# Kernel tuning notes

Measured on AMD Instinct MI355X. Metric: run time of the kernel, lower is better.

## Reference

```python
import jax, jax.numpy as jnp
import numpy as np

EPS = 0.01
BETA = 0.8
GAMMA_A = 0.01
GAMMA_W = 0.01
ALPHA = 1.0
N_UNITS = 128

def setup_inputs() -> dict:
    key = jax.random.key(0)
    ks = jax.random.split(key, 7)
    B, T, D_in, C_out = 512, 1024, 64, 10
    return {
        "x": jax.random.normal(ks[0], (B, T, D_in), dtype=jnp.float32),
        "E_w": jax.random.normal(ks[1], (N_UNITS, D_in), dtype=jnp.float32) / np.sqrt(D_in),
        "E_b": jax.random.normal(ks[2], (N_UNITS,), dtype=jnp.float32) * 0.01,
        "B_p": jax.random.normal(ks[3], (N_UNITS, N_UNITS), dtype=jnp.float32) / N_UNITS,
        "C_p": jax.random.normal(ks[4], (N_UNITS, N_UNITS), dtype=jnp.float32) / N_UNITS,
        "D_w": jax.random.normal(ks[5], (C_out, N_UNITS), dtype=jnp.float32) / np.sqrt(N_UNITS),
        "D_b": jax.random.normal(ks[6], (C_out,), dtype=jnp.float32) * 0.01,
    }

def reference(x, E_w, E_b, B_p, C_p, D_w, D_b):
    B, T, _ = x.shape
    I = jnp.eye(N_UNITS, dtype=x.dtype)
    # Skew/symmetric mixture recurrent matrices (computed once, as in i==0 branch)
    A = BETA * (B_p - B_p.T) + (1.0 - BETA) * (B_p + B_p.T) - GAMMA_A * I
    W = BETA * (C_p - C_p.T) + (1.0 - BETA) * (C_p + C_p.T) - GAMMA_W * I
    # Input projection for all timesteps at once: [T, B, n_units]
    Z = jnp.einsum('bti,ui->tbu', x, E_w) + E_b
    h0 = jnp.zeros((B, N_UNITS), dtype=x.dtype)

    def step(h, z):
        h_update = ALPHA * (h @ A) + jnp.tanh(h @ W + z)
        return h + EPS * h_update, None

    h_final, _ = jax.lax.scan(step, h0, Z)
    return h_final @ D_w.T + D_b
```

## Files before the change

### kernel.cpp

```cpp
#include <hip/hip_runtime.h>

#define EPS_C 0.01f
#define NU    128
#define DIN   64
#define COUT  10
#define TSCALE 2.8853900817779268f

typedef float    f32x4 __attribute__((ext_vector_type(4)));
typedef _Float16 f16x2 __attribute__((ext_vector_type(2)));
typedef _Float16 f16x4 __attribute__((ext_vector_type(4)));
typedef _Float16 f16x8 __attribute__((ext_vector_type(8)));

#define MFMA32(A, B, C) __builtin_amdgcn_mfma_f32_16x16x32_f16((A), (B), (C), 0, 0, 0)
#define BAR() asm volatile("s_waitcnt lgkmcnt(0)\n\ts_barrier" ::: "memory")

__global__ __launch_bounds__(256, 1)
void rnn_core(const float* __restrict__ x,
              const float* __restrict__ E_w, const float* __restrict__ E_b,
              const float* __restrict__ B_p, const float* __restrict__ C_p,
              const float* __restrict__ D_w, const float* __restrict__ D_b,
              float* __restrict__ out, int T)
{
    const int tid  = threadIdx.x;
    const int lane = tid & 63;
    const int w    = tid >> 6;
    const int lid  = lane & 15;
    const int q    = lane >> 4;
    const int g    = blockIdx.x;

    __shared__ __attribute__((aligned(16))) _Float16 xs[2][8 * 1024];
    __shared__ __attribute__((aligned(16))) _Float16 hbuf[2][4][64][8];
    __shared__ float hfin[16][NU + 4];

    f16x8 AT[2][4], WT[2][4], EF[2][2];
    f32x4 ebv[2];
    #pragma unroll
    for (int mt = 0; mt < 2; ++mt) {
        const int m = w * 32 + mt * 16 + lid;
        #pragma unroll
        for (int kt = 0; kt < 4; ++kt) {
            f16x8 fa, fw;
            #pragma unroll
            for (int j = 0; j < 8; ++j) {
                const int k  = kt * 32 + q * 8 + j;
                const float dg = (k == m) ? 0.01f : 0.0f;
                fa[j] = (_Float16)(B_p[k * NU + m] - 0.6f * B_p[m * NU + k] - dg);
                fw[j] = (_Float16)((C_p[k * NU + m] - 0.6f * C_p[m * NU + k] - dg) * TSCALE);
            }
            AT[mt][kt] = fa;  WT[mt][kt] = fw;
        }
        #pragma unroll
        for (int kt = 0; kt < 2; ++kt) {
            f16x8 fe;
            #pragma unroll
            for (int j = 0; j < 8; ++j)
                fe[j] = (_Float16)(E_w[m * DIN + kt * 32 + q * 8 + j] * TSCALE);
            EF[mt][kt] = fe;
        }
        #pragma unroll
        for (int r = 0; r < 4; ++r)
            ebv[mt][r] = E_b[w * 32 + mt * 16 + q * 4 + r] * TSCALE;
    }

    const int bb = tid & 15;
    const int s2 = tid >> 4;
    const float* xrow = x + ((size_t)(g * 16 + bb) * T) * DIN + s2 * 4;
    const int wb2 = (((s2 >> 3) * 64) + (((s2 >> 1) & 3) * 16) + bb) * 16 + (s2 & 1) * 8;

    float4 xg[8];

#define STAGE_WRITE(BUF)                                                      \
    {                                                                         \
        char* base_ = (char*)&xs[(BUF)][0];                                   \
        _Pragma("unroll")                                                     \
        for (int i2 = 0; i2 < 8; ++i2) {                                      \
            float4 v_ = xg[i2];                                               \
            f16x4 h4_;                                                        \
            h4_[0] = (_Float16)v_.x; h4_[1] = (_Float16)v_.y;                 \
            h4_[2] = (_Float16)v_.z; h4_[3] = (_Float16)v_.w;                 \
            *(f16x4*)(base_ + i2 * 2048 + wb2) = h4_;                         \
        }                                                                     \
    }

    ((float4*)&hbuf[0][0][0][0])[tid] = (float4){0.f, 0.f, 0.f, 0.f};
    #pragma unroll
    for (int i = 0; i < 8; ++i)
        xg[i] = *(const float4*)(xrow + (size_t)i * DIN);
    STAGE_WRITE(0)
    __syncthreads();

    char* xsb = (char*)&xs[0][0] + lane * 16;
    char* hrb = (char*)&hbuf[0][0][0][0] + lane * 16;
    char* hwb = (char*)&hbuf[0][0][0][0]
              + (w * 64 + (q >> 1) * 16 + lid) * 16 + (q & 1) * 8;

    f32x4 hf[2] = {{0.f,0.f,0.f,0.f}, {0.f,0.f,0.f,0.f}};
    f32x4 zc0, zc1;
    {
        f16x8 x0 = *(const f16x8*)(xsb);
        f16x8 x1 = *(const f16x8*)(xsb + 1024);
        zc0 = ebv[0];
        zc0 = MFMA32(EF[0][0], x0, zc0);
        zc0 = MFMA32(EF[0][1], x1, zc0);
        zc1 = ebv[1];
        zc1 = MFMA32(EF[1][0], x0, zc1);
        zc1 = MFMA32(EF[1][1], x1, zc1);
    }

    const int nch = T >> 3;
    for (int c = 0; c < nch; ++c) {
        if (c + 1 < nch) {
            const float* xr2 = xrow + (size_t)(c + 1) * 8 * DIN;
            #pragma unroll
            for (int i = 0; i < 8; ++i)
                xg[i] = *(const float4*)(xr2 + (size_t)i * DIN);
        }
        #pragma unroll
        for (int i = 0; i < 8; ++i) {
            const int t  = c * 8 + i;
            const int p  = i & 1;
            const int np = p ^ 1;

            f16x8 hB[4];
            #pragma unroll
            for (int kt = 0; kt < 4; ++kt)
                hB[kt] = *(const f16x8*)(hrb + p * 4096 + kt * 1024);

            int tt = t + 1; if (tt >= T) tt = T - 1;
            char* xb = xsb + ((tt >> 3) & 1) * 16384 + (tt & 7) * 2048;
            f16x8 xfA = *(const f16x8*)(xb);
            f16x8 xfB = *(const f16x8*)(xb + 1024);

            f32x4 wa0 = zc0, wa1 = zc1;
            #pragma unroll
            for (int kt = 0; kt < 4; ++kt) {
                wa0 = MFMA32(WT[0][kt], hB[kt], wa0);
                wa1 = MFMA32(WT[1][kt], hB[kt], wa1);
            }

            float rc[2][4];
            #pragma unroll
            for (int r = 0; r < 4; ++r) {
                rc[0][r] = __builtin_amdgcn_rcpf(__builtin_amdgcn_exp2f(wa0[r]) + 1.0f);
                rc[1][r] = __builtin_amdgcn_rcpf(__builtin_amdgcn_exp2f(wa1[r]) + 1.0f);
            }

            #pragma unroll
            for (int kt = 0; kt < 4; ++kt) {
                hf[0] = MFMA32(AT[0][kt], hB[kt], hf[0]);
                hf[1] = MFMA32(AT[1][kt], hB[kt], hf[1]);
            }
            f32x4 zn0 = ebv[0], zn1 = ebv[1];
            zn0 = MFMA32(EF[0][0], xfA, zn0);
            zn1 = MFMA32(EF[1][0], xfA, zn1);
            zn0 = MFMA32(EF[0][1], xfB, zn0);
            zn1 = MFMA32(EF[1][1], xfB, zn1);

            #pragma unroll
            for (int mt = 0; mt < 2; ++mt) {
                #pragma unroll
                for (int r = 0; r < 4; ++r)
                    hf[mt][r] = __builtin_fmaf(-2.0f, rc[mt][r], hf[mt][r] + 1.0f);
                f16x2 lo = __builtin_bit_cast(f16x2,
                    __builtin_amdgcn_cvt_pkrtz(EPS_C * hf[mt][0], EPS_C * hf[mt][1]));
                f16x2 hi = __builtin_bit_cast(f16x2,
                    __builtin_amdgcn_cvt_pkrtz(EPS_C * hf[mt][2], EPS_C * hf[mt][3]));
                f16x4 nh;
                nh[0] = lo[0]; nh[1] = lo[1]; nh[2] = hi[0]; nh[3] = hi[1];
                *(f16x4*)(hwb + np * 4096 + mt * 512) = nh;
            }
            zc0 = zn0; zc1 = zn1;

            if (i == 5 && c + 1 < nch) STAGE_WRITE((c + 1) & 1)
            BAR();
        }
    }

    #pragma unroll
    for (int mt = 0; mt < 2; ++mt)
        #pragma unroll
        for (int r = 0; r < 4; ++r)
            hfin[lid][w * 32 + mt * 16 + q * 4 + r] = EPS_C * hf[mt][r];
    __syncthreads();

    if (tid < 16 * COUT) {
        const int r  = tid / COUT;
        const int cc = tid - r * COUT;
        float acc = D_b[cc];
        #pragma unroll 8
        for (int u = 0; u < NU; ++u)
            acc = fmaf(hfin[r][u], D_w[cc * NU + u], acc);
        out[((size_t)g * 16 + r) * COUT + cc] = acc;
    }
}

extern "C" void kernel_launch(void* const* d_in, const int* in_sizes, int n_in,
                              void* d_out, int out_size, void* d_ws, size_t ws_size,
                              hipStream_t stream)
{
    const float* x   = (const float*)d_in[0];
    const float* E_w = (const float*)d_in[1];
    const float* E_b = (const float*)d_in[2];
    const float* B_p = (const float*)d_in[3];
    const float* C_p = (const float*)d_in[4];
    const float* D_w = (const float*)d_in[5];
    const float* D_b = (const float*)d_in[6];
    float* out = (float*)d_out;

    const int B  = out_size / COUT;
    const int T  = in_sizes[0] / (B * DIN);
    const int NB = B / 16;

    rnn_core<<<NB, 256, 0, stream>>>(x, E_w, E_b, B_p, C_p, D_w, D_b, out, T);
}
```

Baseline: 586.9 us.

## Split recurrent step across specialized wave groups for W and A matmuls

Doubles the block to eight waves: four compute the tanh branch (W matmul, activation, input projection) and four compute the linear A branch and the state update, exchanging the tanh values through shared memory. The x input is now loaded directly from global memory into registers, prefetched two steps ahead, instead of being staged through shared memory in chunks. The aim is to shorten the serial per-step critical path by running the two matmul chains in parallel. In exchange, each step needs a second barrier and an extra shared-memory round trip.

New measurement: 816.7 us. +39.2%, slower.

```diff
diff --git a/kernel.cpp b/kernel.cpp
--- a/kernel.cpp
+++ b/kernel.cpp
@@ -14,7 +14,19 @@
 #define MFMA32(A, B, C) __builtin_amdgcn_mfma_f32_16x16x32_f16((A), (B), (C), 0, 0, 0)
 #define BAR() asm volatile("s_waitcnt lgkmcnt(0)\n\ts_barrier" ::: "memory")
 
-__global__ __launch_bounds__(256, 1)
+static __device__ inline f16x8 pack8(float4 a, float4 b)
+{
+    f16x2 p0 = __builtin_bit_cast(f16x2, __builtin_amdgcn_cvt_pkrtz(a.x, a.y));
+    f16x2 p1 = __builtin_bit_cast(f16x2, __builtin_amdgcn_cvt_pkrtz(a.z, a.w));
+    f16x2 p2 = __builtin_bit_cast(f16x2, __builtin_amdgcn_cvt_pkrtz(b.x, b.y));
+    f16x2 p3 = __builtin_bit_cast(f16x2, __builtin_amdgcn_cvt_pkrtz(b.z, b.w));
+    f16x8 r;
+    r[0] = p0[0]; r[1] = p0[1]; r[2] = p1[0]; r[3] = p1[1];
+    r[4] = p2[0]; r[5] = p2[1]; r[6] = p3[0]; r[7] = p3[1];
+    return r;
+}
+
+__global__ __launch_bounds__(512, 1)
 void rnn_core(const float* __restrict__ x,
               const float* __restrict__ E_w, const float* __restrict__ E_b,
               const float* __restrict__ B_p, const float* __restrict__ C_p,
@@ -23,164 +35,186 @@
 {
     const int tid  = threadIdx.x;
     const int lane = tid & 63;
-    const int w    = tid >> 6;
+    const int wv   = tid >> 6;
+    const int w4   = wv & 3;
+    const bool isW = wv < 4;
     const int lid  = lane & 15;
     const int q    = lane >> 4;
     const int g    = blockIdx.x;
 
-    __shared__ __attribute__((aligned(16))) _Float16 xs[2][8 * 1024];
     __shared__ __attribute__((aligned(16))) _Float16 hbuf[2][4][64][8];
+    __shared__ __attribute__((aligned(16))) float    thx[4][2][64][4];
     __shared__ float hfin[16][NU + 4];
 
-    f16x8 AT[2][4], WT[2][4], EF[2][2];
+    if (tid < 256)
+        ((float4*)&hbuf[0][0][0][0])[tid] = (float4){0.f, 0.f, 0.f, 0.f};
+
+    char* hrb = (char*)hbuf + lane * 16;
+    char* hwb = (char*)hbuf
+              + (w4 * 64 + (q >> 1) * 16 + lid) * 16 + (q & 1) * 8;
+    char* thb = (char*)thx + w4 * 2048 + lane * 16;
+
+    const int nch = T >> 3;
+
+    const float* xb = x + (size_t)(g * 16 + lid) * T * DIN;
+
+#define LOADX(dst, tt)                                                        \
+    {                                                                         \
+        const float* xp_ = xb + (size_t)(tt) * DIN + q * 8;                   \
+        dst[0] = *(const float4*)(xp_);                                       \
+        dst[1] = *(const float4*)(xp_ + 4);                                   \
+        dst[2] = *(const float4*)(xp_ + 32);                                  \
+        dst[3] = *(const float4*)(xp_ + 36);                                  \
+    }
+
+    f16x8 MT[2][4];
+    f16x8 EF[2][2];
     f32x4 ebv[2];
-    #pragma unroll
-    for (int mt = 0; mt < 2; ++mt) {
-        const int m = w * 32 + mt * 16 + lid;
-        #pragma unroll
-        for (int kt = 0; kt < 4; ++kt) {
-            f16x8 fa, fw;
-            #pragma unroll
-            for (int j = 0; j < 8; ++j) {
-                const int k  = kt * 32 + q * 8 + j;
-                const float dg = (k == m) ? 0.01f : 0.0f;
-                fa[j] = (_Float16)(B_p[k * NU + m] - 0.6f * B_p[m * NU + k] - dg);
-                fw[j] = (_Float16)((C_p[k * NU + m] - 0.6f * C_p[m * NU + k] - dg) * TSCALE);
-            }
-            AT[mt][kt] = fa;  WT[mt][kt] = fw;
+    float4 xr[2][4];
+    f16x8  xf0, xf1;
+    f32x4  zc0, zc1;
+    f32x4  hf[2] = {{0.f,0.f,0.f,0.f}, {0.f,0.f,0.f,0.f}};
+
+    if (isW) {
+        #pragma unroll
+        for (int mt = 0; mt < 2; ++mt) {
+            const int m = w4 * 32 + mt * 16 + lid;
+            #pragma unroll
+            for (int kt = 0; kt < 4; ++kt) {
+                f16x8 fw;
+                #pragma unroll
+                for (int j = 0; j < 8; ++j) {
+                    const int k  = kt * 32 + q * 8 + j;
+                    const float dg = (k == m) ? 0.01f : 0.0f;
+                    fw[j] = (_Float16)((C_p[k * NU + m] - 0.6f * C_p[m * NU + k] - dg) * TSCALE);
+                }
+                MT[mt][kt] = fw;
+            }
+            #pragma unroll
+            for (int kt = 0; kt < 2; ++kt) {
+                f16x8 fe;
+                #pragma unroll
+                for (int j = 0; j < 8; ++j)
+                    fe[j] = (_Float16)(E_w[m * DIN + kt * 32 + q * 8 + j] * TSCALE);
+                EF[mt][kt] = fe;
+            }
+            #pragma unroll
+            for (int r = 0; r < 4; ++r)
+                ebv[mt][r] = E_b[w4 * 32 + mt * 16 + q * 4 + r] * TSCALE;
         }
-        #pragma unroll
-        for (int kt = 0; kt < 2; ++kt) {
-            f16x8 fe;
-            #pragma unroll
-            for (int j = 0; j < 8; ++j)
-                fe[j] = (_Float16)(E_w[m * DIN + kt * 32 + q * 8 + j] * TSCALE);
-            EF[mt][kt] = fe;
+        float4 t0[4];
+        LOADX(t0, 0);
+        f16x8 a0 = pack8(t0[0], t0[1]);
+        f16x8 a1 = pack8(t0[2], t0[3]);
+        zc0 = ebv[0];
+        zc0 = MFMA32(EF[0][0], a0, zc0);
+        zc0 = MFMA32(EF[0][1], a1, zc0);
+        zc1 = ebv[1];
+        zc1 = MFMA32(EF[1][0], a0, zc1);
+        zc1 = MFMA32(EF[1][1], a1, zc1);
+        int t1 = (T > 1) ? 1 : 0;
+        LOADX(t0, t1);
+        xf0 = pack8(t0[0], t0[1]);
+        xf1 = pack8(t0[2], t0[3]);
+        int t2 = (T > 2) ? 2 : T - 1;
+        LOADX(xr[0], t2);
+    } else {
+        #pragma unroll
+        for (int mt = 0; mt < 2; ++mt) {
+            const int m = w4 * 32 + mt * 16 + lid;
+            #pragma unroll
+            for (int kt = 0; kt < 4; ++kt) {
+                f16x8 fa;
+                #pragma unroll
+                for (int j = 0; j < 8; ++j) {
+                    const int k  = kt * 32 + q * 8 + j;
+                    const float dg = (k == m) ? 0.01f : 0.0f;
+                    fa[j] = (_Float16)(B_p[k * NU + m] - 0.6f * B_p[m * NU + k] - dg);
+                }
+                MT[mt][kt] = fa;
+            }
         }
-        #pragma unroll
-        for (int r = 0; r < 4; ++r)
-            ebv[mt][r] = E_b[w * 32 + mt * 16 + q * 4 + r] * TSCALE;
-    }
-
-    const int bb = tid & 15;
-    const int s2 = tid >> 4;
-    const float* xrow = x + ((size_t)(g * 16 + bb) * T) * DIN + s2 * 4;
-    const int wb2 = (((s2 >> 3) * 64) + (((s2 >> 1) & 3) * 16) + bb) * 16 + (s2 & 1) * 8;
-
-    float4 xg[8];
-
-#define STAGE_WRITE(BUF)                                                      \
-    {                                                                         \
-        char* base_ = (char*)&xs[(BUF)][0];                                   \
-        _Pragma("unroll")                                                     \
-        for (int i2 = 0; i2 < 8; ++i2) {                                      \
-            float4 v_ = xg[i2];                                               \
-            f16x4 h4_;                                                        \
-            h4_[0] = (_Float16)v_.x; h4_[1] = (_Float16)v_.y;                 \
-            h4_[2] = (_Float16)v_.z; h4_[3] = (_Float16)v_.w;                 \
-            *(f16x4*)(base_ + i2 * 2048 + wb2) = h4_;                         \
-        }                                                                     \
-    }
-
-    ((float4*)&hbuf[0][0][0][0])[tid] = (float4){0.f, 0.f, 0.f, 0.f};
-    #pragma unroll
-    for (int i = 0; i < 8; ++i)
-        xg[i] = *(const float4*)(xrow + (size_t)i * DIN);
-    STAGE_WRITE(0)
+    }
     __syncthreads();
 
-    char* xsb = (char*)&xs[0][0] + lane * 16;
-    char* hrb = (char*)&hbuf[0][0][0][0] + lane * 16;
-    char* hwb = (char*)&hbuf[0][0][0][0]
-              + (w * 64 + (q >> 1) * 16 + lid) * 16 + (q & 1) * 8;
-
-    f32x4 hf[2] = {{0.f,0.f,0.f,0.f}, {0.f,0.f,0.f,0.f}};
-    f32x4 zc0, zc1;
-    {
-        f16x8 x0 = *(const f16x8*)(xsb);
-        f16x8 x1 = *(const f16x8*)(xsb + 1024);
-        zc0 = ebv[0];
-        zc0 = MFMA32(EF[0][0], x0, zc0);
-        zc0 = MFMA32(EF[0][1], x1, zc0);
-        zc1 = ebv[1];
-        zc1 = MFMA32(EF[1][0], x0, zc1);
-        zc1 = MFMA32(EF[1][1], x1, zc1);
-    }
-
-    const int nch = T >> 3;
     for (int c = 0; c < nch; ++c) {
-        if (c + 1 < nch) {
-            const float* xr2 = xrow + (size_t)(c + 1) * 8 * DIN;
-            #pragma unroll
-            for (int i = 0; i < 8; ++i)
-                xg[i] = *(const float4*)(xr2 + (size_t)i * DIN);
-        }
         #pragma unroll
         for (int i = 0; i < 8; ++i) {
             const int t  = c * 8 + i;
             const int p  = i & 1;
             const int np = p ^ 1;
+            const int s  = i & 1;
 
             f16x8 hB[4];
             #pragma unroll
             for (int kt = 0; kt < 4; ++kt)
                 hB[kt] = *(const f16x8*)(hrb + p * 4096 + kt * 1024);
 
-            int tt = t + 1; if (tt >= T) tt = T - 1;
-            char* xb = xsb + ((tt >> 3) & 1) * 16384 + (tt & 7) * 2048;
-            f16x8 xfA = *(const f16x8*)(xb);
-            f16x8 xfB = *(const f16x8*)(xb + 1024);
-
-            f32x4 wa0 = zc0, wa1 = zc1;
-            #pragma unroll
-            for (int kt = 0; kt < 4; ++kt) {
-                wa0 = MFMA32(WT[0][kt], hB[kt], wa0);
-                wa1 = MFMA32(WT[1][kt], hB[kt], wa1);
-            }
-
-            float rc[2][4];
-            #pragma unroll
-            for (int r = 0; r < 4; ++r) {
-                rc[0][r] = __builtin_amdgcn_rcpf(__builtin_amdgcn_exp2f(wa0[r]) + 1.0f);
-                rc[1][r] = __builtin_amdgcn_rcpf(__builtin_amdgcn_exp2f(wa1[r]) + 1.0f);
-            }
-
-            #pragma unroll
-            for (int kt = 0; kt < 4; ++kt) {
-                hf[0] = MFMA32(AT[0][kt], hB[kt], hf[0]);
-                hf[1] = MFMA32(AT[1][kt], hB[kt], hf[1]);
-            }
-            f32x4 zn0 = ebv[0], zn1 = ebv[1];
-            zn0 = MFMA32(EF[0][0], xfA, zn0);
-            zn1 = MFMA32(EF[1][0], xfA, zn1);
-            zn0 = MFMA32(EF[0][1], xfB, zn0);
-            zn1 = MFMA32(EF[1][1], xfB, zn1);
-
-            #pragma unroll
-            for (int mt = 0; mt < 2; ++mt) {
-                #pragma unroll
-                for (int r = 0; r < 4; ++r)
-                    hf[mt][r] = __builtin_fmaf(-2.0f, rc[mt][r], hf[mt][r] + 1.0f);
-                f16x2 lo = __builtin_bit_cast(f16x2,
-                    __builtin_amdgcn_cvt_pkrtz(EPS_C * hf[mt][0], EPS_C * hf[mt][1]));
-                f16x2 hi = __builtin_bit_cast(f16x2,
-                    __builtin_amdgcn_cvt_pkrtz(EPS_C * hf[mt][2], EPS_C * hf[mt][3]));
-                f16x4 nh;
-                nh[0] = lo[0]; nh[1] = lo[1]; nh[2] = hi[0]; nh[3] = hi[1];
-                *(f16x4*)(hwb + np * 4096 + mt * 512) = nh;
-            }
-            zc0 = zn0; zc1 = zn1;
-
-            if (i == 5 && c + 1 < nch) STAGE_WRITE((c + 1) & 1)
+            if (isW) {
+                f32x4 wa0 = zc0, wa1 = zc1;
+                #pragma unroll
+                for (int kt = 0; kt < 4; ++kt) {
+                    wa0 = MFMA32(MT[0][kt], hB[kt], wa0);
+                    wa1 = MFMA32(MT[1][kt], hB[kt], wa1);
+                }
+                f32x4 th0, th1;
+                #pragma unroll
+                for (int r = 0; r < 4; ++r) {
+                    const float rc0 = __builtin_amdgcn_rcpf(__builtin_amdgcn_exp2f(wa0[r]) + 1.0f);
+                    const float rc1 = __builtin_amdgcn_rcpf(__builtin_amdgcn_exp2f(wa1[r]) + 1.0f);
+                    th0[r] = __builtin_fmaf(-2.0f, rc0, 1.0f);
+                    th1[r] = __builtin_fmaf(-2.0f, rc1, 1.0f);
+                }
+                *(f32x4*)(thb)        = th0;
+                *(f32x4*)(thb + 1024) = th1;
+            } else {
+                #pragma unroll
+                for (int kt = 0; kt < 4; ++kt) {
+                    hf[0] = MFMA32(MT[0][kt], hB[kt], hf[0]);
+                    hf[1] = MFMA32(MT[1][kt], hB[kt], hf[1]);
+                }
+            }
+            BAR();
+
+            if (isW) {
+                f32x4 zn0 = ebv[0], zn1 = ebv[1];
+                zn0 = MFMA32(EF[0][0], xf0, zn0);
+                zn1 = MFMA32(EF[1][0], xf0, zn1);
+                zn0 = MFMA32(EF[0][1], xf1, zn0);
+                zn1 = MFMA32(EF[1][1], xf1, zn1);
+                zc0 = zn0; zc1 = zn1;
+
+                xf0 = pack8(xr[s][0], xr[s][1]);
+                xf1 = pack8(xr[s][2], xr[s][3]);
+                int t3 = t + 3; if (t3 >= T) t3 = T - 1;
+                LOADX(xr[s ^ 1], t3);
+            } else {
+                f32x4 th0 = *(const f32x4*)(thb);
+                f32x4 th1 = *(const f32x4*)(thb + 1024);
+                hf[0] += th0;
+                hf[1] += th1;
+                #pragma unroll
+                for (int mt = 0; mt < 2; ++mt) {
+                    f16x2 lo = __builtin_bit_cast(f16x2,
+                        __builtin_amdgcn_cvt_pkrtz(EPS_C * hf[mt][0], EPS_C * hf[mt][1]));
+                    f16x2 hi = __builtin_bit_cast(f16x2,
+                        __builtin_amdgcn_cvt_pkrtz(EPS_C * hf[mt][2], EPS_C * hf[mt][3]));
+                    f16x4 nh;
+                    nh[0] = lo[0]; nh[1] = lo[1]; nh[2] = hi[0]; nh[3] = hi[1];
+                    *(f16x4*)(hwb + np * 4096 + mt * 512) = nh;
+                }
+            }
             BAR();
         }
     }
 
-    #pragma unroll
-    for (int mt = 0; mt < 2; ++mt)
-        #pragma unroll
-        for (int r = 0; r < 4; ++r)
-            hfin[lid][w * 32 + mt * 16 + q * 4 + r] = EPS_C * hf[mt][r];
+    if (!isW) {
+        #pragma unroll
+        for (int mt = 0; mt < 2; ++mt)
+            #pragma unroll
+            for (int r = 0; r < 4; ++r)
+                hfin[lid][w4 * 32 + mt * 16 + q * 4 + r] = EPS_C * hf[mt][r];
+    }
     __syncthreads();
 
     if (tid < 16 * COUT) {
@@ -211,5 +245,5 @@
     const int T  = in_sizes[0] / (B * DIN);
     const int NB = B / 16;
 
-    rnn_core<<<NB, 256, 0, stream>>>(x, E_w, E_b, B_p, C_p, D_w, D_b, out, T);
+    rnn_core<<<NB, 512, 0, stream>>>(x, E_w, E_b, B_p, C_p, D_w, D_b, out, T);
 }
```
